# Optimization experiments

Hardware: AMD Instinct MI355X
Metric: run time of the kernel (lower is better)

The kernel has to match this reference:

```python
import jax, jax.numpy as jnp
import numpy as np

H = 32  # hidden size

def setup_inputs() -> dict:
    key = jax.random.key(0)
    ks = jax.random.split(key, 12)
    B, T = 64, 16384
    s = 0.1
    return {
        "x": jax.random.normal(ks[0], (B, T, 1), dtype=jnp.float32),
        "h_state": jax.random.normal(ks[1], (2, B, H), dtype=jnp.float32),
        "W_ih0": jax.random.normal(ks[2], (H, 1), dtype=jnp.float32) * s,
        "W_hh0": jax.random.normal(ks[3], (H, H), dtype=jnp.float32) * s,
        "b_ih0": jax.random.normal(ks[4], (H,), dtype=jnp.float32) * s,
        "b_hh0": jax.random.normal(ks[5], (H,), dtype=jnp.float32) * s,
        "W_ih1": jax.random.normal(ks[6], (H, H), dtype=jnp.float32) * s,
        "W_hh1": jax.random.normal(ks[7], (H, H), dtype=jnp.float32) * s,
        "b_ih1": jax.random.normal(ks[8], (H,), dtype=jnp.float32) * s,
        "b_hh1": jax.random.normal(ks[9], (H,), dtype=jnp.float32) * s,
        "W_out": jax.random.normal(ks[10], (1, H), dtype=jnp.float32) * s,
        "b_out": jax.random.normal(ks[11], (1,), dtype=jnp.float32) * s,
    }

def reference(x, h_state, W_ih0, W_hh0, b_ih0, b_hh0, W_ih1, W_hh1, b_ih1, b_hh1, W_out, b_out):
    # x: [B,T,1], h_state: [2,B,H]. PyTorch RNN (tanh):
    #   h_t = tanh(W_ih x_t + b_ih + W_hh h_{t-1} + b_hh)
    # Precompute the input projection for layer 0 outside the scan (memory-bound part).
    pre0 = jnp.einsum('bti,hi->tbh', x, W_ih0) + (b_ih0 + b_hh0)  # [T,B,H]
    b1 = b_ih1 + b_hh1

    def step(carry, p0):
        h0, h1 = carry
        h0n = jnp.tanh(p0 + h0 @ W_hh0.T)
        h1n = jnp.tanh(h0n @ W_ih1.T + b1 + h1 @ W_hh1.T)
        return (h0n, h1n), h1n

    (hf0, hf1), ys = jax.lax.scan(step, (h_state[0], h_state[1]), pre0)
    r_out = jnp.transpose(ys, (1, 0, 2)).reshape(-1, H)  # [B*T, H] (batch_first view)
    outs = r_out @ W_out.T + b_out                        # [B*T, 1]
    h_final = jnp.stack([hf0, hf1])                       # [2,B,H]
    return outs, h_final
```

## Files before the change

### kernel.cpp

```cpp
#include <hip/hip_runtime.h>


#define T_LEN 16384
#define B_SZ  64
#define NW    (T_LEN / 32)
#define TSC   2.885390082f

#if __has_builtin(__builtin_amdgcn_exp2f)
#define EXP2(x) __builtin_amdgcn_exp2f(x)
#else
#define EXP2(x) exp2f(x)
#endif

typedef _Float16 h2 __attribute__((ext_vector_type(2)));

__device__ __forceinline__ float rl(float v, int lane) {
  return __int_as_float(__builtin_amdgcn_readlane(__float_as_int(v), lane));
}

__device__ __forceinline__ h2 rl_h2(h2 v, int lane) {
  int o = __builtin_amdgcn_readlane(__builtin_bit_cast(int, v), lane);
  return __builtin_bit_cast(h2, o);
}

__device__ __forceinline__ h2 bperm_h2(int byteaddr, h2 v) {
  int o = __builtin_amdgcn_ds_bpermute(byteaddr, __builtin_bit_cast(int, v));
  return __builtin_bit_cast(h2, o);
}

__device__ __forceinline__ float pair_swap(float v) {
  int t = __builtin_amdgcn_update_dpp(0, __float_as_int(v), 0xB1, 0xF, 0xF, true);
  return __int_as_float(t);
}

__device__ __forceinline__ float tanh_pre(float v) {
  float e = EXP2(v);
  return fmaf(-2.f, __builtin_amdgcn_rcpf(e + 1.f), 1.f);
}

#if __has_builtin(__builtin_amdgcn_fdot2)
#define FDOT2(a, b, c) __builtin_amdgcn_fdot2((a), (b), (c), false)
#else
#define FDOT2(a, b, c) \
  fmaf((float)(a).x, (float)(b).x, fmaf((float)(a).y, (float)(b).y, (c)))
#endif

__device__ __forceinline__ h2 pack_state(float hcur) {
  float hsw = pair_swap(hcur);
#if __has_builtin(__builtin_amdgcn_cvt_pkrtz)
  return __builtin_bit_cast(h2, __builtin_amdgcn_cvt_pkrtz(hcur, hsw));
#else
  h2 p; p.x = (_Float16)hcur; p.y = (_Float16)hsw; return p;
#endif
}

#define BCASTMIX(dst, src_pk)                                  \
  _Pragma("unroll")                                            \
  for (int j_ = 0; j_ < 8; ++j_) {                             \
    (dst)[j_]     = rl_h2((src_pk), 2 * j_);                   \
    (dst)[j_ + 8] = bperm_h2(64 + 8 * j_, (src_pk));           \
  }

__device__ __forceinline__ float dot32h(const h2* w, const h2* hb, float seed) {
  float a0 = seed, a1 = 0.f, a2 = 0.f, a3 = 0.f;
#pragma unroll
  for (int j = 0; j < 4; ++j) {
    a0 = FDOT2(w[4 * j + 0], hb[4 * j + 0], a0);
    a1 = FDOT2(w[4 * j + 1], hb[4 * j + 1], a1);
    a2 = FDOT2(w[4 * j + 2], hb[4 * j + 2], a2);
    a3 = FDOT2(w[4 * j + 3], hb[4 * j + 3], a3);
  }
  return (a0 + a1) + (a2 + a3);
}

__global__ __launch_bounds__(128, 1) void rnn2_kernel(
    const float* __restrict__ x,    const float* __restrict__ hs,
    const float* __restrict__ Wih0, const float* __restrict__ Whh0,
    const float* __restrict__ bih0, const float* __restrict__ bhh0,
    const float* __restrict__ Wih1, const float* __restrict__ Whh1,
    const float* __restrict__ bih1, const float* __restrict__ bhh1,
    const float* __restrict__ Wout, const float* __restrict__ bout,
    float* __restrict__ out)
{
  __shared__ __align__(16) float uwin[2][1024];
  __shared__ __align__(16) float scratch[1024];

  const int  tid = (int)threadIdx.x;
  const int  wv  = tid >> 6;
  const int  m   = tid & 63;
  const int  r   = m & 31;
  const bool hi  = (m >= 32);
  const int  b   = (int)blockIdx.x;

  const float* pw = (wv == 0) ? (hi ? (Wih1 + r * 32) : (Whh0 + r * 32))
                              : (hi ? Wout : (Whh1 + r * 32));
  const float wsc = (wv == 0) ? TSC : (hi ? 1.f : TSC);
  h2 w[16];
#pragma unroll
  for (int k = 0; k < 8; ++k) {
    float4 q = ((const float4*)pw)[k];
    w[2 * k].x     = (_Float16)(q.x * wsc);
    w[2 * k].y     = (_Float16)(q.y * wsc);
    w[2 * k + 1].x = (_Float16)(q.z * wsc);
    w[2 * k + 1].y = (_Float16)(q.w * wsc);
  }

  float xw = 0.f, binv = 0.f;
  if (wv == 0) {
    if (hi) binv = TSC * (bih1[r] + bhh1[r]);
    else  { binv = TSC * (bih0[r] + bhh0[r]); xw = TSC * Wih0[r]; }
  }
  const float bo = bout[0];

  float hcur = (wv == 0) ? hs[b * 32 + r] : hs[2048 + b * 32 + r];

  float* up0 = hi ? &uwin[0][r] : &scratch[r];
  float* up1 = hi ? &uwin[1][r] : &scratch[r];

  const float* xb   = x + (size_t)b * T_LEN;
  float*       outp = out + (size_t)b * T_LEN;
  float*       hf   = out + (size_t)B_SZ * T_LEN;

  float obuf = 0.f;
  float xcur = 0.f;
  if (wv == 0) xcur = xb[m];

  for (int wdx = 0; wdx <= NW; ++wdx) {
    if (wv == 0) {
      if (wdx < NW) {
        float xnext = 0.f;
        if (wdx + 1 < NW) {
          int xi = 32 * (wdx + 1) + m; if (xi > T_LEN - 1) xi = T_LEN - 1;
          xnext = xb[xi];
        }
        float* up = (wdx & 1) ? up1 : up0;
#pragma unroll 8
        for (int t2 = 0; t2 < 32; ++t2) {
          h2 hpk = pack_state(hcur);
          h2 hb[16];
          BCASTMIX(hb, hpk);
          float xv   = rl(xcur, t2);
          float seed = fmaf(xv, xw, binv);
          float acc  = dot32h(w, hb, seed);
          up[t2 * 32] = acc;
          hcur = tanh_pre(acc);
        }
        xcur = xnext;
      }
    } else {
      if (wdx >= 1) {
        const int wb = wdx - 1;
        const float* ub = &uwin[wb & 1][r];
        float uval = ub[0];
#pragma unroll 8
        for (int t2 = 0; t2 < 32; ++t2) {
          const int t = 32 * wb - 1 + t2;
          h2 hpk = pack_state(hcur);
          h2 hb[16];
          BCASTMIX(hb, hpk);
          float sB  = hi ? 0.f : uval;
          float acc = dot32h(w, hb, sB);
          float unext = ub[((t2 + 1) & 31) * 32];
          float h1n = tanh_pre(acc);
          obuf = (m == 32 + t2) ? acc : obuf;
          if (t >= 0) hcur = h1n;
          uval = unext;
        }
        const int idx = 32 * wb - 2 + r;
        if (hi && idx >= 0) outp[idx] = obuf + bo;
      }
    }
    __syncthreads();
  }

  if (wv == 0) {
    h2 hpk = pack_state(hcur);
    h2 hb[16];
    BCASTMIX(hb, hpk);
    float acc = dot32h(w, hb, binv);
    if (hi) uwin[0][r] = acc;
    else    hf[b * 32 + r] = hcur;
  }
  __syncthreads();

  if (wv == 1) {
    float uT = uwin[0][r];
    h2 hpk = pack_state(hcur);
    h2 hb[16];
    BCASTMIX(hb, hpk);
    float acc = dot32h(w, hb, hi ? 0.f : uT);
    if (m == 32) outp[T_LEN - 2] = acc + bo;
    float h1T = tanh_pre(acc);
    h2 hpk2 = pack_state(h1T);
    h2 hb2[16];
    BCASTMIX(hb2, hpk2);
    float acc2 = dot32h(w, hb2, 0.f);
    if (m == 32) outp[T_LEN - 1] = acc2 + bo;
    if (!hi) hf[2048 + b * 32 + r] = h1T;
  }
}

extern "C" void kernel_launch(void* const* d_in, const int* in_sizes, int n_in,
                              void* d_out, int out_size, void* d_ws, size_t ws_size,
                              hipStream_t stream) {
  rnn2_kernel<<<dim3(B_SZ), dim3(128), 0, stream>>>(
      (const float*)d_in[0],  (const float*)d_in[1],  (const float*)d_in[2],
      (const float*)d_in[3],  (const float*)d_in[4],  (const float*)d_in[5],
      (const float*)d_in[6],  (const float*)d_in[7],  (const float*)d_in[8],
      (const float*)d_in[9],  (const float*)d_in[10], (const float*)d_in[11],
      (float*)d_out);
}
```

Measured before the change: 1.836 ms.

## Interleave two batch sequences per block to hide serial recurrence latency

Each block now processes two independent batch rows instead of one, interleaving their recurrent steps so the broadcast, dot-product and tanh dependency chains of one sequence can overlap with the other. Scheduling barriers are inserted to force this interleaving, and the grid is halved to 32 blocks. The aim is to fill the latency bubbles in the strictly serial per-step chain. In exchange, per-wave instruction count per step doubles, register pressure rises, and half as many CUs are used.

```diff
diff --git a/kernel.cpp b/kernel.cpp
--- a/kernel.cpp
+++ b/kernel.cpp
@@ -12,6 +12,12 @@
 #define EXP2(x) exp2f(x)
 #endif
 
+#if __has_builtin(__builtin_amdgcn_sched_barrier)
+#define SCHED_FENCE() __builtin_amdgcn_sched_barrier(0)
+#else
+#define SCHED_FENCE()
+#endif
+
 typedef _Float16 h2 __attribute__((ext_vector_type(2)));
 
 __device__ __forceinline__ float rl(float v, int lane) {
@@ -31,11 +37,6 @@
 __device__ __forceinline__ float pair_swap(float v) {
   int t = __builtin_amdgcn_update_dpp(0, __float_as_int(v), 0xB1, 0xF, 0xF, true);
   return __int_as_float(t);
-}
-
-__device__ __forceinline__ float tanh_pre(float v) {
-  float e = EXP2(v);
-  return fmaf(-2.f, __builtin_amdgcn_rcpf(e + 1.f), 1.f);
 }
 
 #if __has_builtin(__builtin_amdgcn_fdot2)
@@ -61,15 +62,20 @@
     (dst)[j_ + 8] = bperm_h2(64 + 8 * j_, (src_pk));           \
   }
 
+#define DOT8(A0, A1, A2, A3, W, HB, B)                         \
+  A0 = FDOT2((W)[4*(B)+0], (HB)[4*(B)+0], A0);                 \
+  A1 = FDOT2((W)[4*(B)+1], (HB)[4*(B)+1], A1);                 \
+  A2 = FDOT2((W)[4*(B)+2], (HB)[4*(B)+2], A2);                 \
+  A3 = FDOT2((W)[4*(B)+3], (HB)[4*(B)+3], A3);                 \
+  A0 = FDOT2((W)[4*(B)+4], (HB)[4*(B)+4], A0);                 \
+  A1 = FDOT2((W)[4*(B)+5], (HB)[4*(B)+5], A1);                 \
+  A2 = FDOT2((W)[4*(B)+6], (HB)[4*(B)+6], A2);                 \
+  A3 = FDOT2((W)[4*(B)+7], (HB)[4*(B)+7], A3);
+
 __device__ __forceinline__ float dot32h(const h2* w, const h2* hb, float seed) {
   float a0 = seed, a1 = 0.f, a2 = 0.f, a3 = 0.f;
-#pragma unroll
-  for (int j = 0; j < 4; ++j) {
-    a0 = FDOT2(w[4 * j + 0], hb[4 * j + 0], a0);
-    a1 = FDOT2(w[4 * j + 1], hb[4 * j + 1], a1);
-    a2 = FDOT2(w[4 * j + 2], hb[4 * j + 2], a2);
-    a3 = FDOT2(w[4 * j + 3], hb[4 * j + 3], a3);
-  }
+  DOT8(a0, a1, a2, a3, w, hb, 0);
+  DOT8(a0, a1, a2, a3, w, hb, 2);
   return (a0 + a1) + (a2 + a3);
 }
 
@@ -82,7 +88,7 @@
     const float* __restrict__ Wout, const float* __restrict__ bout,
     float* __restrict__ out)
 {
-  __shared__ __align__(16) float uwin[2][1024];
+  __shared__ __align__(16) float uwin[2][2][1024];
   __shared__ __align__(16) float scratch[1024];
 
   const int  tid = (int)threadIdx.x;
@@ -90,7 +96,8 @@
   const int  m   = tid & 63;
   const int  r   = m & 31;
   const bool hi  = (m >= 32);
-  const int  b   = (int)blockIdx.x;
+  const int  b0  = (int)blockIdx.x * 2;
+  const int  b1  = b0 + 1;
 
   const float* pw = (wv == 0) ? (hi ? (Wih1 + r * 32) : (Whh0 + r * 32))
                               : (hi ? Wout : (Whh1 + r * 32));
@@ -112,98 +119,170 @@
   }
   const float bo = bout[0];
 
-  float hcur = (wv == 0) ? hs[b * 32 + r] : hs[2048 + b * 32 + r];
-
-  float* up0 = hi ? &uwin[0][r] : &scratch[r];
-  float* up1 = hi ? &uwin[1][r] : &scratch[r];
-
-  const float* xb   = x + (size_t)b * T_LEN;
-  float*       outp = out + (size_t)b * T_LEN;
+  float hc0 = (wv == 0) ? hs[b0 * 32 + r] : hs[2048 + b0 * 32 + r];
+  float hc1 = (wv == 0) ? hs[b1 * 32 + r] : hs[2048 + b1 * 32 + r];
+
+  float* upA[2][2];
+  upA[0][0] = hi ? &uwin[0][0][r] : &scratch[r];
+  upA[0][1] = hi ? &uwin[0][1][r] : &scratch[r];
+  upA[1][0] = hi ? &uwin[1][0][r] : &scratch[r];
+  upA[1][1] = hi ? &uwin[1][1][r] : &scratch[r];
+
+  const float* xb0  = x + (size_t)b0 * T_LEN;
+  const float* xb1  = x + (size_t)b1 * T_LEN;
+  float*       op0  = out + (size_t)b0 * T_LEN;
+  float*       op1  = out + (size_t)b1 * T_LEN;
   float*       hf   = out + (size_t)B_SZ * T_LEN;
 
-  float obuf = 0.f;
-  float xcur = 0.f;
-  if (wv == 0) xcur = xb[m];
+  float ob0 = 0.f, ob1 = 0.f;
+  float xc0 = 0.f, xc1 = 0.f;
+  if (wv == 0) { xc0 = xb0[m]; xc1 = xb1[m]; }
 
   for (int wdx = 0; wdx <= NW; ++wdx) {
     if (wv == 0) {
       if (wdx < NW) {
-        float xnext = 0.f;
+        float xn0 = 0.f, xn1 = 0.f;
         if (wdx + 1 < NW) {
           int xi = 32 * (wdx + 1) + m; if (xi > T_LEN - 1) xi = T_LEN - 1;
-          xnext = xb[xi];
+          xn0 = xb0[xi]; xn1 = xb1[xi];
         }
-        float* up = (wdx & 1) ? up1 : up0;
-#pragma unroll 8
+        float* up0 = upA[0][wdx & 1];
+        float* up1 = upA[1][wdx & 1];
+#pragma unroll 4
         for (int t2 = 0; t2 < 32; ++t2) {
-          h2 hpk = pack_state(hcur);
-          h2 hb[16];
-          BCASTMIX(hb, hpk);
-          float xv   = rl(xcur, t2);
-          float seed = fmaf(xv, xw, binv);
-          float acc  = dot32h(w, hb, seed);
-          up[t2 * 32] = acc;
-          hcur = tanh_pre(acc);
+          float xv0 = rl(xc0, t2);
+          float xv1 = rl(xc1, t2);
+          float sd0 = fmaf(xv0, xw, binv);
+          float sd1 = fmaf(xv1, xw, binv);
+          h2 hp0 = pack_state(hc0);
+          h2 hp1 = pack_state(hc1);
+          SCHED_FENCE();
+          h2 hb0[16]; BCASTMIX(hb0, hp0);
+          SCHED_FENCE();
+          h2 hb1[16]; BCASTMIX(hb1, hp1);
+          SCHED_FENCE();
+          float a00 = sd0, a01 = 0.f, a02 = 0.f, a03 = 0.f;
+          DOT8(a00, a01, a02, a03, w, hb0, 0);
+          SCHED_FENCE();
+          float a10 = sd1, a11 = 0.f, a12 = 0.f, a13 = 0.f;
+          DOT8(a10, a11, a12, a13, w, hb1, 0);
+          SCHED_FENCE();
+          DOT8(a00, a01, a02, a03, w, hb0, 2);
+          float ac0 = (a00 + a01) + (a02 + a03);
+          up0[t2 * 32] = ac0;
+          SCHED_FENCE();
+          DOT8(a10, a11, a12, a13, w, hb1, 2);
+          float ac1 = (a10 + a11) + (a12 + a13);
+          up1[t2 * 32] = ac1;
+          float e0 = EXP2(ac0);
+          SCHED_FENCE();
+          float e1 = EXP2(ac1);
+          hc0 = fmaf(-2.f, __builtin_amdgcn_rcpf(e0 + 1.f), 1.f);
+          SCHED_FENCE();
+          hc1 = fmaf(-2.f, __builtin_amdgcn_rcpf(e1 + 1.f), 1.f);
         }
-        xcur = xnext;
+        xc0 = xn0; xc1 = xn1;
       }
     } else {
       if (wdx >= 1) {
         const int wb = wdx - 1;
-        const float* ub = &uwin[wb & 1][r];
-        float uval = ub[0];
-#pragma unroll 8
+        const float* ub0 = &uwin[0][wb & 1][r];
+        const float* ub1 = &uwin[1][wb & 1][r];
+        float uv0 = ub0[0];
+        float uv1 = ub1[0];
+#pragma unroll 4
         for (int t2 = 0; t2 < 32; ++t2) {
           const int t = 32 * wb - 1 + t2;
-          h2 hpk = pack_state(hcur);
-          h2 hb[16];
-          BCASTMIX(hb, hpk);
-          float sB  = hi ? 0.f : uval;
-          float acc = dot32h(w, hb, sB);
-          float unext = ub[((t2 + 1) & 31) * 32];
-          float h1n = tanh_pre(acc);
-          obuf = (m == 32 + t2) ? acc : obuf;
-          if (t >= 0) hcur = h1n;
-          uval = unext;
+          h2 hp0 = pack_state(hc0);
+          h2 hp1 = pack_state(hc1);
+          float un0 = ub0[((t2 + 1) & 31) * 32];
+          float un1 = ub1[((t2 + 1) & 31) * 32];
+          SCHED_FENCE();
+          h2 hb0[16]; BCASTMIX(hb0, hp0);
+          SCHED_FENCE();
+          h2 hb1[16]; BCASTMIX(hb1, hp1);
+          SCHED_FENCE();
+          float a00 = hi ? 0.f : uv0, a01 = 0.f, a02 = 0.f, a03 = 0.f;
+          DOT8(a00, a01, a02, a03, w, hb0, 0);
+          SCHED_FENCE();
+          float a10 = hi ? 0.f : uv1, a11 = 0.f, a12 = 0.f, a13 = 0.f;
+          DOT8(a10, a11, a12, a13, w, hb1, 0);
+          SCHED_FENCE();
+          DOT8(a00, a01, a02, a03, w, hb0, 2);
+          float ac0 = (a00 + a01) + (a02 + a03);
+          ob0 = (m == 32 + t2) ? ac0 : ob0;
+          SCHED_FENCE();
+          DOT8(a10, a11, a12, a13, w, hb1, 2);
+          float ac1 = (a10 + a11) + (a12 + a13);
+          ob1 = (m == 32 + t2) ? ac1 : ob1;
+          float e0 = EXP2(ac0);
+          SCHED_FENCE();
+          float e1 = EXP2(ac1);
+          float h0n = fmaf(-2.f, __builtin_amdgcn_rcpf(e0 + 1.f), 1.f);
+          if (t >= 0) hc0 = h0n;
+          uv0 = un0;
+          SCHED_FENCE();
+          float h1n = fmaf(-2.f, __builtin_amdgcn_rcpf(e1 + 1.f), 1.f);
+          if (t >= 0) hc1 = h1n;
+          uv1 = un1;
         }
         const int idx = 32 * wb - 2 + r;
-        if (hi && idx >= 0) outp[idx] = obuf + bo;
+        if (hi && idx >= 0) { op0[idx] = ob0 + bo; op1[idx] = ob1 + bo; }
       }
     }
     __syncthreads();
   }
 
   if (wv == 0) {
-    h2 hpk = pack_state(hcur);
-    h2 hb[16];
-    BCASTMIX(hb, hpk);
-    float acc = dot32h(w, hb, binv);
-    if (hi) uwin[0][r] = acc;
-    else    hf[b * 32 + r] = hcur;
+    h2 hp0 = pack_state(hc0);
+    h2 hb0[16]; BCASTMIX(hb0, hp0);
+    float a0 = dot32h(w, hb0, binv);
+    if (hi) uwin[0][0][r] = a0;
+    else    hf[b0 * 32 + r] = hc0;
+    h2 hp1 = pack_state(hc1);
+    h2 hb1[16]; BCASTMIX(hb1, hp1);
+    float a1 = dot32h(w, hb1, binv);
+    if (hi) uwin[1][0][r] = a1;
+    else    hf[b1 * 32 + r] = hc1;
   }
   __syncthreads();
 
   if (wv == 1) {
-    float uT = uwin[0][r];
-    h2 hpk = pack_state(hcur);
-    h2 hb[16];
-    BCASTMIX(hb, hpk);
-    float acc = dot32h(w, hb, hi ? 0.f : uT);
-    if (m == 32) outp[T_LEN - 2] = acc + bo;
-    float h1T = tanh_pre(acc);
-    h2 hpk2 = pack_state(h1T);
-    h2 hb2[16];
-    BCASTMIX(hb2, hpk2);
-    float acc2 = dot32h(w, hb2, 0.f);
-    if (m == 32) outp[T_LEN - 1] = acc2 + bo;
-    if (!hi) hf[2048 + b * 32 + r] = h1T;
+    {
+      float uT = uwin[0][0][r];
+      h2 hp = pack_state(hc0);
+      h2 hb[16]; BCASTMIX(hb, hp);
+      float acc = dot32h(w, hb, hi ? 0.f : uT);
+      if (m == 32) op0[T_LEN - 2] = acc + bo;
+      float e = EXP2(acc);
+      float h1T = fmaf(-2.f, __builtin_amdgcn_rcpf(e + 1.f), 1.f);
+      h2 hp2 = pack_state(h1T);
+      h2 hb2[16]; BCASTMIX(hb2, hp2);
+      float acc2 = dot32h(w, hb2, 0.f);
+      if (m == 32) op0[T_LEN - 1] = acc2 + bo;
+      if (!hi) hf[2048 + b0 * 32 + r] = h1T;
+    }
+    {
+      float uT = uwin[1][0][r];
+      h2 hp = pack_state(hc1);
+      h2 hb[16]; BCASTMIX(hb, hp);
+      float acc = dot32h(w, hb, hi ? 0.f : uT);
+      if (m == 32) op1[T_LEN - 2] = acc + bo;
+      float e = EXP2(acc);
+      float h1T = fmaf(-2.f, __builtin_amdgcn_rcpf(e + 1.f), 1.f);
+      h2 hp2 = pack_state(h1T);
+      h2 hb2[16]; BCASTMIX(hb2, hp2);
+      float acc2 = dot32h(w, hb2, 0.f);
+      if (m == 32) op1[T_LEN - 1] = acc2 + bo;
+      if (!hi) hf[2048 + b1 * 32 + r] = h1T;
+    }
   }
 }
 
 extern "C" void kernel_launch(void* const* d_in, const int* in_sizes, int n_in,
                               void* d_out, int out_size, void* d_ws, size_t ws_size,
                               hipStream_t stream) {
-  rnn2_kernel<<<dim3(B_SZ), dim3(128), 0, stream>>>(
+  rnn2_kernel<<<dim3(B_SZ / 2), dim3(128), 0, stream>>>(
       (const float*)d_in[0],  (const float*)d_in[1],  (const float*)d_in[2],
       (const float*)d_in[3],  (const float*)d_in[4],  (const float*)d_in[5],
       (const float*)d_in[6],  (const float*)d_in[7],  (const float*)d_in[8],
```

Result: slower. 3.569 ms (+94.3%).
